# Performance work log

Measured on AMD Instinct MI355X. Metric: run time of the kernel, lower is better.

## Reference

```python
import jax, jax.numpy as jnp
import numpy as np

WEIGHT = 0.1
EPS = 1e-8


def setup_inputs() -> dict:
    key = jax.random.key(0)
    # [B, 3, D, H, W] deformation field
    deformation_field = jax.random.normal(key, (2, 3, 192, 192, 192), dtype=jnp.float32)
    return {"deformation_field": deformation_field}


def reference(deformation_field):
    f = deformation_field
    # jnp.gradient matches torch.gradient defaults: 2nd-order central interior,
    # 1st-order one-sided differences at the edges, unit spacing.
    grad_x = jnp.gradient(f, axis=2)
    grad_y = jnp.gradient(f, axis=3)
    grad_z = jnp.gradient(f, axis=4)

    divergence = grad_x[:, 0:1] + grad_y[:, 1:2] + grad_z[:, 2:3]
    divergence_loss = jnp.mean(divergence ** 2)

    curl_x = grad_z[:, 1:2] - grad_y[:, 2:3]
    curl_y = grad_x[:, 2:3] - grad_z[:, 0:1]
    curl_z = grad_y[:, 0:1] - grad_x[:, 1:2]
    curl_magnitude = jnp.sqrt(curl_x ** 2 + curl_y ** 2 + curl_z ** 2 + EPS)
    curl_loss = jnp.mean(curl_magnitude)

    return WEIGHT * (divergence_loss + curl_loss)
```

## Files before the change

### kernel.cpp

```cpp
#include <hip/hip_runtime.h>


#define DEP 192
#define HGT 192
#define WID 192
#define NB  2

constexpr int SD = HGT * WID;
constexpr int SC = DEP * SD;
constexpr int SB = 3 * SC;
constexpr int W4 = WID / 4;
constexpr int DSEG = 8;
constexpr int NSEG = DEP / DSEG;
constexpr int NG   = NB * NSEG * HGT * W4;
constexpr int NBLK = NG / 256;
constexpr float SCALE = (float)(0.1 / (double)((long long)NB * DEP * HGT * WID));
constexpr float EPS_C = 1e-8f;

struct V4 { float v[4]; };
__device__ __forceinline__ V4 ld(const float* p) {
    const float4 t = *(const float4*)p;
    V4 r; r.v[0] = t.x; r.v[1] = t.y; r.v[2] = t.z; r.v[3] = t.w; return r;
}

__global__ __launch_bounds__(256, 3) void gcl_kernel(const float* __restrict__ f,
                                                     float* __restrict__ ws) {
    const int g = blockIdx.x * 256 + threadIdx.x;

    int w4 = g % W4;
    int t  = g / W4;
    int h  = t % HGT;
    t /= HGT;
    int ds = t % NSEG;
    int b  = t / NSEG;
    const int w  = w4 * 4;
    const int d0 = ds * DSEG;

    const int   hmi = (h > 0) ? h - 1 : 0;
    const int   hpi = (h < HGT - 1) ? h + 1 : HGT - 1;
    const float sy  = (h == 0 || h == HGT - 1) ? 1.0f : 0.5f;
    const int   dhm = (hmi - h) * WID;
    const int   dhp = (hpi - h) * WID;
    const int   loff = (w > 0) ? -1 : 0;
    const int   roff = (w4 < W4 - 1) ? 4 : 3;

    const float* base = f + b * SB + h * WID + w;

    V4 prev[3], cur[3], nxt[3], vhm[3], vhp[3];
    float lf[3], rt[3];

    const int pm = (d0 > 0) ? d0 - 1 : 0;
#pragma unroll
    for (int c = 0; c < 3; ++c) {
        const float* pc = base + c * SC;
        prev[c] = ld(pc + pm * SD);
        cur[c]  = ld(pc + d0 * SD);
        nxt[c]  = ld(pc + (d0 + 1) * SD);
        vhm[c]  = ld(pc + d0 * SD + dhm);
        vhp[c]  = ld(pc + d0 * SD + dhp);
        lf[c]   = (pc + d0 * SD)[loff];
        rt[c]   = (pc + d0 * SD)[roff];
    }

    float local = 0.f;

#pragma unroll
    for (int s = 0; s < DSEG; ++s) {
        const int d = d0 + s;

        V4 nn[3], nhm[3], nhp[3];
        float nl[3], nr[3];
        if (s < DSEG - 1) {
            const int dn = d + 1;
            const int d2 = (d + 2 < DEP) ? d + 2 : DEP - 1;
#pragma unroll
            for (int c = 0; c < 3; ++c) {
                const float* pc = base + c * SC;
                nn[c]  = ld(pc + d2 * SD);
                nhm[c] = ld(pc + dn * SD + dhm);
                nhp[c] = ld(pc + dn * SD + dhp);
                nl[c]  = (pc + dn * SD)[loff];
                nr[c]  = (pc + dn * SD)[roff];
            }
        }

        const float sx = (d == 0 || d == DEP - 1) ? 1.0f : 0.5f;
        float gx[3][4], gy[3][4], gz[3][4];
#pragma unroll
        for (int c = 0; c < 3; ++c) {
#pragma unroll
            for (int j = 0; j < 4; ++j) {
                gx[c][j] = sx * (nxt[c].v[j] - prev[c].v[j]);
                gy[c][j] = sy * (vhp[c].v[j] - vhm[c].v[j]);
            }
            gz[c][0] = (w == 0)       ? (cur[c].v[1] - cur[c].v[0])
                                      : 0.5f * (cur[c].v[1] - lf[c]);
            gz[c][1] = 0.5f * (cur[c].v[2] - cur[c].v[0]);
            gz[c][2] = 0.5f * (cur[c].v[3] - cur[c].v[1]);
            gz[c][3] = (w4 == W4 - 1) ? (cur[c].v[3] - cur[c].v[2])
                                      : 0.5f * (rt[c] - cur[c].v[2]);
        }
#pragma unroll
        for (int j = 0; j < 4; ++j) {
            const float dv = gx[0][j] + gy[1][j] + gz[2][j];
            const float cx = gz[1][j] - gy[2][j];
            const float cy = gx[2][j] - gz[0][j];
            const float cz = gy[0][j] - gx[1][j];
            local += dv * dv + sqrtf(cx * cx + cy * cy + cz * cz + EPS_C);
        }

        if (s < DSEG - 1) {
#pragma unroll
            for (int c = 0; c < 3; ++c) {
                prev[c] = cur[c]; cur[c] = nxt[c]; nxt[c] = nn[c];
                vhm[c] = nhm[c]; vhp[c] = nhp[c];
                lf[c] = nl[c];   rt[c] = nr[c];
            }
        }
    }

#pragma unroll
    for (int off = 32; off > 0; off >>= 1)
        local += __shfl_down(local, off, 64);

    __shared__ float wsum[4];
    const int lane = threadIdx.x & 63;
    const int wv   = threadIdx.x >> 6;
    if (lane == 0) wsum[wv] = local;
    __syncthreads();
    if (threadIdx.x == 0)
        ws[blockIdx.x] = wsum[0] + wsum[1] + wsum[2] + wsum[3];
}

__global__ __launch_bounds__(256) void gcl_reduce(const float* __restrict__ ws,
                                                  float* __restrict__ out) {
    float s = 0.f;
    for (int i = threadIdx.x; i < NBLK; i += 256) s += ws[i];
#pragma unroll
    for (int off = 32; off > 0; off >>= 1)
        s += __shfl_down(s, off, 64);
    __shared__ float wsum[4];
    const int lane = threadIdx.x & 63;
    const int wv   = threadIdx.x >> 6;
    if (lane == 0) wsum[wv] = s;
    __syncthreads();
    if (threadIdx.x == 0)
        out[0] = (wsum[0] + wsum[1] + wsum[2] + wsum[3]) * SCALE;
}

extern "C" void kernel_launch(void* const* d_in, const int* in_sizes, int n_in,
                              void* d_out, int out_size, void* d_ws, size_t ws_size,
                              hipStream_t stream) {
    const float* f = (const float*)d_in[0];
    float* out = (float*)d_out;
    float* ws  = (float*)d_ws;
    gcl_kernel<<<dim3(NBLK), dim3(256), 0, stream>>>(f, ws);
    gcl_reduce<<<dim3(1), dim3(256), 0, stream>>>(ws, out);
}
```

Baseline: 240.4 us.

## Tile H/W in shared memory to reuse neighbor rows and columns across threads

Replaces per-thread global loads of the h±1 rows and w±1 edge values with a 16x64 block tile staged in LDS plus a halo, advanced one depth slice at a time. Only halo threads fetch the extra rows and columns from global memory, which cuts redundant global and L2 traffic. The depth segment length also grows from 8 to 12. In exchange it adds two __syncthreads per slice and LDS reads and writes, and halo threads diverge from the rest.

Result: slower. 383.0 us (+59.3%).

```diff
diff --git a/kernel.cpp b/kernel.cpp
--- a/kernel.cpp
+++ b/kernel.cpp
@@ -9,58 +9,103 @@
 constexpr int SD = HGT * WID;
 constexpr int SC = DEP * SD;
 constexpr int SB = 3 * SC;
-constexpr int W4 = WID / 4;
-constexpr int DSEG = 8;
-constexpr int NSEG = DEP / DSEG;
-constexpr int NG   = NB * NSEG * HGT * W4;
-constexpr int NBLK = NG / 256;
+constexpr int TH   = 16;
+constexpr int TW4  = 16;
+constexpr int TW   = TW4 * 4;
+constexpr int DSEG = 12;
+constexpr int NDS  = DEP / DSEG;
+constexpr int NHB  = HGT / TH;
+constexpr int NWB  = WID / TW;
+constexpr int NBLK = NB * NDS * NHB * NWB;
+constexpr int ROWF = (TW4 + 1) * 4;
 constexpr float SCALE = (float)(0.1 / (double)((long long)NB * DEP * HGT * WID));
 constexpr float EPS_C = 1e-8f;
 
 struct V4 { float v[4]; };
-__device__ __forceinline__ V4 ld(const float* p) {
+__device__ __forceinline__ V4 ld4(const float* p) {
     const float4 t = *(const float4*)p;
     V4 r; r.v[0] = t.x; r.v[1] = t.y; r.v[2] = t.z; r.v[3] = t.w; return r;
 }
+__device__ __forceinline__ void st4(float* p, const V4& a) {
+    *(float4*)p = make_float4(a.v[0], a.v[1], a.v[2], a.v[3]);
+}
+__device__ __forceinline__ V4 ld4s(const float* p) {
+    const float4 t = *(const float4*)p;
+    V4 r; r.v[0] = t.x; r.v[1] = t.y; r.v[2] = t.z; r.v[3] = t.w; return r;
+}
 
 __global__ __launch_bounds__(256, 3) void gcl_kernel(const float* __restrict__ f,
                                                      float* __restrict__ ws) {
-    const int g = blockIdx.x * 256 + threadIdx.x;
-
-    int w4 = g % W4;
-    int t  = g / W4;
-    int h  = t % HGT;
-    t /= HGT;
-    int ds = t % NSEG;
-    int b  = t / NSEG;
-    const int w  = w4 * 4;
-    const int d0 = ds * DSEG;
-
-    const int   hmi = (h > 0) ? h - 1 : 0;
-    const int   hpi = (h < HGT - 1) ? h + 1 : HGT - 1;
+    __shared__ float cen[3][TH + 2][ROWF];
+    __shared__ float lcol[3][TH], rcol[3][TH];
+
+    const int tid = threadIdx.x;
+    const int tx = tid & 15;
+    const int ty = tid >> 4;
+
+    int bid = blockIdx.x;
+    const int wb = bid % NWB; bid /= NWB;
+    const int hb = bid % NHB; bid /= NHB;
+    const int dsg = bid % NDS;
+    const int b = bid / NDS;
+
+    const int h0 = hb * TH, w0 = wb * TW, d0 = dsg * DSEG;
+    const int h = h0 + ty;
+    const int w = w0 + tx * 4;
+
     const float sy  = (h == 0 || h == HGT - 1) ? 1.0f : 0.5f;
-    const int   dhm = (hmi - h) * WID;
-    const int   dhp = (hpi - h) * WID;
-    const int   loff = (w > 0) ? -1 : 0;
-    const int   roff = (w4 < W4 - 1) ? 4 : 3;
-
-    const float* base = f + b * SB + h * WID + w;
-
-    V4 prev[3], cur[3], nxt[3], vhm[3], vhp[3];
-    float lf[3], rt[3];
-
+    const float s0w = (w == 0) ? 1.0f : 0.5f;
+    const float s3w = (w + 3 == WID - 1) ? 1.0f : 0.5f;
+
+    const bool isTop = (ty == 0), isBot = (ty == TH - 1);
+    const bool isL = (tx == 0),  isR = (tx == TW4 - 1);
+    const bool isRow = isTop || isBot;
+    const bool isCol = isL || isR;
+    const int hrow = isTop ? (h0 > 0 ? h0 - 1 : 0)
+                           : (h0 + TH < HGT ? h0 + TH : HGT - 1);
+    const int wcol = isL ? (w0 > 0 ? w0 - 1 : 0)
+                         : (w0 + TW < WID ? w0 + TW : WID - 1);
+
+    const float* fb = f + b * SB;
     const int pm = (d0 > 0) ? d0 - 1 : 0;
+
+    V4 prev[3], cur[3], nxt[3], nn[3];
+    V4 hrowA[3], hrowB[3];
+    float hcolA[3], hcolB[3];
+
 #pragma unroll
     for (int c = 0; c < 3; ++c) {
-        const float* pc = base + c * SC;
-        prev[c] = ld(pc + pm * SD);
-        cur[c]  = ld(pc + d0 * SD);
-        nxt[c]  = ld(pc + (d0 + 1) * SD);
-        vhm[c]  = ld(pc + d0 * SD + dhm);
-        vhp[c]  = ld(pc + d0 * SD + dhp);
-        lf[c]   = (pc + d0 * SD)[loff];
-        rt[c]   = (pc + d0 * SD)[roff];
-    }
+        const float* pcen = fb + c * SC + h * WID + w;
+        prev[c] = ld4(pcen + pm * SD);
+        cur[c]  = ld4(pcen + d0 * SD);
+        nxt[c]  = ld4(pcen + (d0 + 1) * SD);
+    }
+    V4 hrow0[3]; float hcol0[3];
+    if (isRow) {
+#pragma unroll
+        for (int c = 0; c < 3; ++c) {
+            const float* pr = fb + c * SC + hrow * WID + w;
+            hrow0[c] = ld4(pr + d0 * SD);
+            hrowA[c] = ld4(pr + (d0 + 1) * SD);
+        }
+    }
+    if (isCol) {
+#pragma unroll
+        for (int c = 0; c < 3; ++c) {
+            const float* pq = fb + c * SC + h * WID + wcol;
+            hcol0[c] = pq[d0 * SD];
+            hcolA[c] = pq[(d0 + 1) * SD];
+        }
+    }
+#pragma unroll
+    for (int c = 0; c < 3; ++c) {
+        st4(&cen[c][ty + 1][tx * 4], cur[c]);
+        if (isTop) st4(&cen[c][0][tx * 4], hrow0[c]);
+        if (isBot) st4(&cen[c][TH + 1][tx * 4], hrow0[c]);
+        if (isL) lcol[c][ty] = hcol0[c];
+        if (isR) rcol[c][ty] = hcol0[c];
+    }
+    __syncthreads();
 
     float local = 0.f;
 
@@ -68,19 +113,20 @@
     for (int s = 0; s < DSEG; ++s) {
         const int d = d0 + s;
 
-        V4 nn[3], nhm[3], nhp[3];
-        float nl[3], nr[3];
         if (s < DSEG - 1) {
-            const int dn = d + 1;
             const int d2 = (d + 2 < DEP) ? d + 2 : DEP - 1;
 #pragma unroll
-            for (int c = 0; c < 3; ++c) {
-                const float* pc = base + c * SC;
-                nn[c]  = ld(pc + d2 * SD);
-                nhm[c] = ld(pc + dn * SD + dhm);
-                nhp[c] = ld(pc + dn * SD + dhp);
-                nl[c]  = (pc + dn * SD)[loff];
-                nr[c]  = (pc + dn * SD)[roff];
+            for (int c = 0; c < 3; ++c)
+                nn[c] = ld4(fb + c * SC + d2 * SD + h * WID + w);
+            if (isRow) {
+#pragma unroll
+                for (int c = 0; c < 3; ++c)
+                    hrowB[c] = ld4(fb + c * SC + d2 * SD + hrow * WID + w);
+            }
+            if (isCol) {
+#pragma unroll
+                for (int c = 0; c < 3; ++c)
+                    hcolB[c] = (fb + c * SC + d2 * SD + h * WID)[wcol];
             }
         }
 
@@ -88,17 +134,19 @@
         float gx[3][4], gy[3][4], gz[3][4];
 #pragma unroll
         for (int c = 0; c < 3; ++c) {
+            const V4 hm = ld4s(&cen[c][ty][tx * 4]);
+            const V4 hp = ld4s(&cen[c][ty + 2][tx * 4]);
+            const float lv = isL ? lcol[c][ty] : cen[c][ty + 1][tx * 4 - 1];
+            const float rv = isR ? rcol[c][ty] : cen[c][ty + 1][tx * 4 + 4];
 #pragma unroll
             for (int j = 0; j < 4; ++j) {
                 gx[c][j] = sx * (nxt[c].v[j] - prev[c].v[j]);
-                gy[c][j] = sy * (vhp[c].v[j] - vhm[c].v[j]);
-            }
-            gz[c][0] = (w == 0)       ? (cur[c].v[1] - cur[c].v[0])
-                                      : 0.5f * (cur[c].v[1] - lf[c]);
+                gy[c][j] = sy * (hp.v[j] - hm.v[j]);
+            }
+            gz[c][0] = s0w * (cur[c].v[1] - lv);
             gz[c][1] = 0.5f * (cur[c].v[2] - cur[c].v[0]);
             gz[c][2] = 0.5f * (cur[c].v[3] - cur[c].v[1]);
-            gz[c][3] = (w4 == W4 - 1) ? (cur[c].v[3] - cur[c].v[2])
-                                      : 0.5f * (rt[c] - cur[c].v[2]);
+            gz[c][3] = s3w * (rv - cur[c].v[2]);
         }
 #pragma unroll
         for (int j = 0; j < 4; ++j) {
@@ -110,11 +158,20 @@
         }
 
         if (s < DSEG - 1) {
+            __syncthreads();
+#pragma unroll
+            for (int c = 0; c < 3; ++c) {
+                st4(&cen[c][ty + 1][tx * 4], nxt[c]);
+                if (isTop) st4(&cen[c][0][tx * 4], hrowA[c]);
+                if (isBot) st4(&cen[c][TH + 1][tx * 4], hrowA[c]);
+                if (isL) lcol[c][ty] = hcolA[c];
+                if (isR) rcol[c][ty] = hcolA[c];
+            }
+            __syncthreads();
 #pragma unroll
             for (int c = 0; c < 3; ++c) {
                 prev[c] = cur[c]; cur[c] = nxt[c]; nxt[c] = nn[c];
-                vhm[c] = nhm[c]; vhp[c] = nhp[c];
-                lf[c] = nl[c];   rt[c] = nr[c];
+                hrowA[c] = hrowB[c]; hcolA[c] = hcolB[c];
             }
         }
     }
@@ -124,11 +181,11 @@
         local += __shfl_down(local, off, 64);
 
     __shared__ float wsum[4];
-    const int lane = threadIdx.x & 63;
-    const int wv   = threadIdx.x >> 6;
+    const int lane = tid & 63;
+    const int wv   = tid >> 6;
     if (lane == 0) wsum[wv] = local;
     __syncthreads();
-    if (threadIdx.x == 0)
+    if (tid == 0)
         ws[blockIdx.x] = wsum[0] + wsum[1] + wsum[2] + wsum[3];
 }
 
```

## Map one wavefront to a full row pair with lane shuffles for W-neighbours

Applied to the files above, without the earlier changes.

Each wavefront now covers a whole 192-wide row, with 3 floats per lane. It processes two adjacent H rows so the vertical neighbour loads are shared: four row loads per plane instead of six. The W-direction neighbours now come from cross-lane shuffles instead of extra scalar loads, and the depth segment grows from 8 to 12 planes. The float3 loads are not 16-byte aligned, which may lower load efficiency. The grid also becomes much smaller (NB*16*24 blocks), which could hurt occupancy and latency hiding. The sqrt is swapped for the hardware builtin.

Measured after the change: 234.0 us. 1.03x faster.

```diff
diff --git a/kernel.cpp b/kernel.cpp
--- a/kernel.cpp
+++ b/kernel.cpp
@@ -9,57 +9,59 @@
 constexpr int SD = HGT * WID;
 constexpr int SC = DEP * SD;
 constexpr int SB = 3 * SC;
-constexpr int W4 = WID / 4;
-constexpr int DSEG = 8;
+constexpr int DSEG = 12;
 constexpr int NSEG = DEP / DSEG;
-constexpr int NG   = NB * NSEG * HGT * W4;
-constexpr int NBLK = NG / 256;
+constexpr int RPB  = 4;
+constexpr int NRPG = (HGT / 2) / RPB;
+constexpr int NBLK = NB * NSEG * NRPG;
 constexpr float SCALE = (float)(0.1 / (double)((long long)NB * DEP * HGT * WID));
 constexpr float EPS_C = 1e-8f;
 
-struct V4 { float v[4]; };
-__device__ __forceinline__ V4 ld(const float* p) {
-    const float4 t = *(const float4*)p;
-    V4 r; r.v[0] = t.x; r.v[1] = t.y; r.v[2] = t.z; r.v[3] = t.w; return r;
+struct V3 { float x, y, z; };
+__device__ __forceinline__ V3 ld3(const float* p) {
+    const float3 t = *(const float3*)p;
+    V3 r; r.x = t.x; r.y = t.y; r.z = t.z; return r;
 }
 
 __global__ __launch_bounds__(256, 3) void gcl_kernel(const float* __restrict__ f,
                                                      float* __restrict__ ws) {
-    const int g = blockIdx.x * 256 + threadIdx.x;
+    const int tid  = threadIdx.x;
+    const int lane = tid & 63;
+    const int wv   = tid >> 6;
 
-    int w4 = g % W4;
-    int t  = g / W4;
-    int h  = t % HGT;
-    t /= HGT;
-    int ds = t % NSEG;
-    int b  = t / NSEG;
-    const int w  = w4 * 4;
-    const int d0 = ds * DSEG;
+    int bid = blockIdx.x;
+    const int rpg = bid % NRPG; bid /= NRPG;
+    const int dsg = bid % NSEG;
+    const int b   = bid / NSEG;
 
-    const int   hmi = (h > 0) ? h - 1 : 0;
-    const int   hpi = (h < HGT - 1) ? h + 1 : HGT - 1;
-    const float sy  = (h == 0 || h == HGT - 1) ? 1.0f : 0.5f;
-    const int   dhm = (hmi - h) * WID;
-    const int   dhp = (hpi - h) * WID;
-    const int   loff = (w > 0) ? -1 : 0;
-    const int   roff = (w4 < W4 - 1) ? 4 : 3;
+    const int h0 = (rpg * RPB + wv) * 2;
+    const int h1 = h0 + 1;
+    const int w  = lane * 3;
+    const int d0 = dsg * DSEG;
 
-    const float* base = f + b * SB + h * WID + w;
+    const int hmrow = (h0 > 0) ? h0 - 1 : 0;
+    const int hprow = (h1 < HGT - 1) ? h1 + 1 : HGT - 1;
+    const float sy0 = (h0 == 0) ? 1.f : 0.5f;
+    const float sy1 = (h1 == HGT - 1) ? 1.f : 0.5f;
+    const float s0w = (lane == 0) ? 1.f : 0.5f;
+    const float s2w = (lane == 63) ? 1.f : 0.5f;
 
-    V4 prev[3], cur[3], nxt[3], vhm[3], vhp[3];
-    float lf[3], rt[3];
+    const float* base = f + b * SB + w;
+    const int r0 = h0 * WID, r1 = h1 * WID, rm = hmrow * WID, rp = hprow * WID;
 
+    V3 prev[3][2], cur[3][2], nxt[3][2], hm[3], hp[3];
     const int pm = (d0 > 0) ? d0 - 1 : 0;
 #pragma unroll
     for (int c = 0; c < 3; ++c) {
         const float* pc = base + c * SC;
-        prev[c] = ld(pc + pm * SD);
-        cur[c]  = ld(pc + d0 * SD);
-        nxt[c]  = ld(pc + (d0 + 1) * SD);
-        vhm[c]  = ld(pc + d0 * SD + dhm);
-        vhp[c]  = ld(pc + d0 * SD + dhp);
-        lf[c]   = (pc + d0 * SD)[loff];
-        rt[c]   = (pc + d0 * SD)[roff];
+        prev[c][0] = ld3(pc + pm * SD + r0);
+        prev[c][1] = ld3(pc + pm * SD + r1);
+        cur[c][0]  = ld3(pc + d0 * SD + r0);
+        cur[c][1]  = ld3(pc + d0 * SD + r1);
+        nxt[c][0]  = ld3(pc + (d0 + 1) * SD + r0);
+        nxt[c][1]  = ld3(pc + (d0 + 1) * SD + r1);
+        hm[c]      = ld3(pc + d0 * SD + rm);
+        hp[c]      = ld3(pc + d0 * SD + rp);
     }
 
     float local = 0.f;
@@ -68,53 +70,62 @@
     for (int s = 0; s < DSEG; ++s) {
         const int d = d0 + s;
 
-        V4 nn[3], nhm[3], nhp[3];
-        float nl[3], nr[3];
+        V3 nn[3][2], nhm[3], nhp[3];
         if (s < DSEG - 1) {
             const int dn = d + 1;
             const int d2 = (d + 2 < DEP) ? d + 2 : DEP - 1;
 #pragma unroll
             for (int c = 0; c < 3; ++c) {
                 const float* pc = base + c * SC;
-                nn[c]  = ld(pc + d2 * SD);
-                nhm[c] = ld(pc + dn * SD + dhm);
-                nhp[c] = ld(pc + dn * SD + dhp);
-                nl[c]  = (pc + dn * SD)[loff];
-                nr[c]  = (pc + dn * SD)[roff];
+                nn[c][0] = ld3(pc + d2 * SD + r0);
+                nn[c][1] = ld3(pc + d2 * SD + r1);
+                nhm[c]   = ld3(pc + dn * SD + rm);
+                nhp[c]   = ld3(pc + dn * SD + rp);
             }
         }
 
-        const float sx = (d == 0 || d == DEP - 1) ? 1.0f : 0.5f;
-        float gx[3][4], gy[3][4], gz[3][4];
+        const float sx = (d == 0 || d == DEP - 1) ? 1.f : 0.5f;
+
 #pragma unroll
-        for (int c = 0; c < 3; ++c) {
+        for (int r = 0; r < 2; ++r) {
+            const float syr = r ? sy1 : sy0;
+            float gx[3][3], gy[3][3], gz[3][3];
 #pragma unroll
-            for (int j = 0; j < 4; ++j) {
-                gx[c][j] = sx * (nxt[c].v[j] - prev[c].v[j]);
-                gy[c][j] = sy * (vhp[c].v[j] - vhm[c].v[j]);
+            for (int c = 0; c < 3; ++c) {
+                gx[c][0] = sx * (nxt[c][r].x - prev[c][r].x);
+                gx[c][1] = sx * (nxt[c][r].y - prev[c][r].y);
+                gx[c][2] = sx * (nxt[c][r].z - prev[c][r].z);
+                const V3 lo = r ? cur[c][0] : hm[c];
+                const V3 hi = r ? hp[c]     : cur[c][1];
+                gy[c][0] = syr * (hi.x - lo.x);
+                gy[c][1] = syr * (hi.y - lo.y);
+                gy[c][2] = syr * (hi.z - lo.z);
+                float lv = __shfl_up(cur[c][r].z, 1, 64);
+                float rv = __shfl_down(cur[c][r].x, 1, 64);
+                if (lane == 0)  lv = cur[c][r].x;
+                if (lane == 63) rv = cur[c][r].z;
+                gz[c][0] = s0w * (cur[c][r].y - lv);
+                gz[c][1] = 0.5f * (cur[c][r].z - cur[c][r].x);
+                gz[c][2] = s2w * (rv - cur[c][r].y);
             }
-            gz[c][0] = (w == 0)       ? (cur[c].v[1] - cur[c].v[0])
-                                      : 0.5f * (cur[c].v[1] - lf[c]);
-            gz[c][1] = 0.5f * (cur[c].v[2] - cur[c].v[0]);
-            gz[c][2] = 0.5f * (cur[c].v[3] - cur[c].v[1]);
-            gz[c][3] = (w4 == W4 - 1) ? (cur[c].v[3] - cur[c].v[2])
-                                      : 0.5f * (rt[c] - cur[c].v[2]);
-        }
 #pragma unroll
-        for (int j = 0; j < 4; ++j) {
-            const float dv = gx[0][j] + gy[1][j] + gz[2][j];
-            const float cx = gz[1][j] - gy[2][j];
-            const float cy = gx[2][j] - gz[0][j];
-            const float cz = gy[0][j] - gx[1][j];
-            local += dv * dv + sqrtf(cx * cx + cy * cy + cz * cz + EPS_C);
+            for (int j = 0; j < 3; ++j) {
+                const float dv = gx[0][j] + gy[1][j] + gz[2][j];
+                const float cx = gz[1][j] - gy[2][j];
+                const float cy = gx[2][j] - gz[0][j];
+                const float cz = gy[0][j] - gx[1][j];
+                local += dv * dv +
+                         __builtin_amdgcn_sqrtf(cx * cx + cy * cy + cz * cz + EPS_C);
+            }
         }
 
         if (s < DSEG - 1) {
 #pragma unroll
             for (int c = 0; c < 3; ++c) {
-                prev[c] = cur[c]; cur[c] = nxt[c]; nxt[c] = nn[c];
-                vhm[c] = nhm[c]; vhp[c] = nhp[c];
-                lf[c] = nl[c];   rt[c] = nr[c];
+                prev[c][0] = cur[c][0]; prev[c][1] = cur[c][1];
+                cur[c][0]  = nxt[c][0]; cur[c][1]  = nxt[c][1];
+                nxt[c][0]  = nn[c][0];  nxt[c][1]  = nn[c][1];
+                hm[c] = nhm[c]; hp[c] = nhp[c];
             }
         }
     }
@@ -124,11 +135,9 @@
         local += __shfl_down(local, off, 64);
 
     __shared__ float wsum[4];
-    const int lane = threadIdx.x & 63;
-    const int wv   = threadIdx.x >> 6;
     if (lane == 0) wsum[wv] = local;
     __syncthreads();
-    if (threadIdx.x == 0)
+    if (tid == 0)
         ws[blockIdx.x] = wsum[0] + wsum[1] + wsum[2] + wsum[3];
 }
 
```
